# Kernel optimization log

Measured on AMD Instinct MI355X. Metric: run time of the kernel, lower is better.

The kernel has to match this reference:

```python
import jax, jax.numpy as jnp
import numpy as np

HIDDEN = 1024
HEADS = 16
HEAD_DIM = HIDDEN // HEADS


def setup_inputs() -> dict:
    key = jax.random.key(0)
    k_x, k_wa, k_ba, k_wp, k_bp = jax.random.split(key, 5)
    x = jax.random.normal(k_x, (2, 2048, HIDDEN), dtype=jnp.float32)
    s_a = 1.0 / np.sqrt(HIDDEN)
    # torch Linear default init ~ U(-1/sqrt(fan_in), 1/sqrt(fan_in)); stored as [in, out]
    W_attn = jax.random.uniform(k_wa, (HIDDEN, 3 * HIDDEN), jnp.float32, -s_a, s_a)
    b_attn = jax.random.uniform(k_ba, (3 * HIDDEN,), jnp.float32, -s_a, s_a)
    W_proj = jax.random.uniform(k_wp, (HIDDEN, HIDDEN), jnp.float32, -s_a, s_a)
    b_proj = jax.random.uniform(k_bp, (HIDDEN,), jnp.float32, -s_a, s_a)
    return {"x": x, "W_attn": W_attn, "b_attn": b_attn, "W_proj": W_proj, "b_proj": b_proj}


def reference(x, W_attn, b_attn, W_proj, b_proj):
    B, S, D = x.shape
    H, Hd = HEADS, HEAD_DIM
    qkv = x @ W_attn + b_attn                     # [B, S, 3D]
    q, k, v = jnp.split(qkv, 3, axis=-1)
    # [B, H, S, Hd]
    q = q.reshape(B, S, H, Hd).transpose(0, 2, 1, 3)
    k = k.reshape(B, S, H, Hd).transpose(0, 2, 1, 3)
    v = v.reshape(B, S, H, Hd).transpose(0, 2, 1, 3)
    scale = 1.0 / np.sqrt(Hd).astype(np.float32)
    scores = jnp.einsum('bhqd,bhkd->bhqk', q, k) * scale   # [B, H, S, S]
    causal = jnp.triu(jnp.ones((S, S), dtype=bool), k=1)   # True above diagonal
    scores = jnp.where(causal, -jnp.inf, scores)
    probs = jax.nn.softmax(scores, axis=-1)
    # dropout p=0.0 -> identity (eval-mode equivalent)
    ctx = jnp.einsum('bhqk,bhkd->bhqd', probs, v)           # [B, H, S, Hd]
    ctx = ctx.transpose(0, 2, 1, 3).reshape(B, S, D)
    return ctx @ W_proj + b_proj
```

## Files before the change

### kernel.cpp

```cpp
#include <hip/hip_runtime.h>
#include <hip/hip_bf16.h>
#include <stdint.h>

#define HID 1024
#define NH 16
#define HD 64
#define SEQ 2048
#define BATCH 2
#define M_TOT 4096
#define QSCALE 0.18033688011112042f

typedef __attribute__((ext_vector_type(8))) short short8;
typedef __attribute__((ext_vector_type(4))) float f32x4;
typedef __attribute__((ext_vector_type(16))) float f32x16;
typedef __hip_bfloat16 bf16;

__device__ __forceinline__ void load_lds16(const void* g, void* l) {
  __builtin_amdgcn_global_load_lds(
      (const __attribute__((address_space(1))) unsigned int*)g,
      (__attribute__((address_space(3))) unsigned int*)l, 16, 0, 0);
}

__device__ __forceinline__ unsigned short f2bf_bits(float f) {
  __hip_bfloat16 h = __float2bfloat16(f);
  return *reinterpret_cast<unsigned short*>(&h);
}
__device__ __forceinline__ unsigned pack2bf(float a, float b) {
  return (unsigned)f2bf_bits(a) | ((unsigned)f2bf_bits(b) << 16);
}
__device__ __forceinline__ unsigned cvt_pk_bf16(float a, float b) {
  unsigned r;
  asm("v_cvt_pk_bf16_f32 %0, %1, %2" : "=v"(r) : "v"(a), "v"(b));
  return r;
}

__global__ void cvt_f32_to_bf16(const float* __restrict__ in,
                                bf16* __restrict__ out, int n4) {
  int i = blockIdx.x * blockDim.x + threadIdx.x;
  if (i >= n4) return;
  float4 v = reinterpret_cast<const float4*>(in)[i];
  ushort4 o;
  o.x = f2bf_bits(v.x); o.y = f2bf_bits(v.y);
  o.z = f2bf_bits(v.z); o.w = f2bf_bits(v.w);
  reinterpret_cast<ushort4*>(out)[i] = o;
}

__global__ void transpose_cvt2(const float* __restrict__ Wa, bf16* __restrict__ WTa,
                               const float* __restrict__ Wp, bf16* __restrict__ WTp) {
  __shared__ float tile[32][33];
  int bx = blockIdx.x;
  const float* W; bf16* WT; int N;
  if (bx < 96) { W = Wa; WT = WTa; N = 3072; }
  else         { W = Wp; WT = WTp; N = 1024; bx -= 96; }
  const int K = 1024;
  int n0 = bx * 32, k0 = blockIdx.y * 32;
  int tx = threadIdx.x, ty = threadIdx.y;
#pragma unroll
  for (int i = 0; i < 32; i += 8)
    tile[ty + i][tx] = W[(size_t)(k0 + ty + i) * N + n0 + tx];
  __syncthreads();
#pragma unroll
  for (int i = 0; i < 32; i += 8)
    WT[(size_t)(n0 + ty + i) * K + k0 + tx] = __float2bfloat16(tile[tx][ty + i]);
}

template <int EPI>
__global__ __launch_bounds__(256, 2)
void gemm128(const bf16* __restrict__ A, const bf16* __restrict__ BT,
             const float* __restrict__ bias,
             bf16* __restrict__ Qo, bf16* __restrict__ Ko, bf16* __restrict__ Vo,
             float* __restrict__ Fo) {
  const int Kdim = 1024;
  __shared__ bf16 As[128 * 64];
  __shared__ bf16 Bs[128 * 64];
  const int tid = threadIdx.x;
  const int wid = tid >> 6, lane = tid & 63;
  const int m0 = blockIdx.x * 128;
  const int n0 = blockIdx.y * 128;
  const int wrow = (wid >> 1) * 64, wcol = (wid & 1) * 64;

  f32x4 acc[4][4];
#pragma unroll
  for (int rb = 0; rb < 4; ++rb)
#pragma unroll
    for (int cb = 0; cb < 4; ++cb)
      acc[rb][cb] = (f32x4){0.f, 0.f, 0.f, 0.f};

  const int lr = lane >> 3;
  const int cc = lane & 7;
  const int lc = cc * 8;
  const int fr = lane & 15, fk = (lane >> 4) * 8;

  for (int kt = 0; kt < Kdim / 64; ++kt) {
    __syncthreads();
#pragma unroll
    for (int t = 0; t < 4; ++t) {
      int i = wid * 4 + t;
      int row = i * 8 + lr;
      load_lds16(A + (size_t)(m0 + row) * Kdim + kt * 64 + lc, (char*)As + i * 1024);
      load_lds16(BT + (size_t)(n0 + row) * Kdim + kt * 64 + lc, (char*)Bs + i * 1024);
    }
    __syncthreads();

    short8 af[4][2], bf_[4][2];
#pragma unroll
    for (int rb = 0; rb < 4; ++rb)
#pragma unroll
      for (int kk = 0; kk < 2; ++kk) {
        af[rb][kk] = *(const short8*)&As[(wrow + rb * 16 + fr) * 64 + kk * 32 + fk];
        bf_[rb][kk] = *(const short8*)&Bs[(wcol + rb * 16 + fr) * 64 + kk * 32 + fk];
      }
#pragma unroll
    for (int rb = 0; rb < 4; ++rb)
#pragma unroll
      for (int cb = 0; cb < 4; ++cb)
#pragma unroll
        for (int kk = 0; kk < 2; ++kk)
          acc[rb][cb] = __builtin_amdgcn_mfma_f32_16x16x32_bf16(
              af[rb][kk], bf_[cb][kk], acc[rb][cb], 0, 0, 0);
  }

  const int fg = (lane >> 4) * 4;
  float bv[4];
#pragma unroll
  for (int cb = 0; cb < 4; ++cb) bv[cb] = bias[n0 + wcol + cb * 16 + fr];

  if (EPI == 0) {
    __syncthreads();
    char* ep = (wid < 2 ? (char*)As : (char*)Bs) + (wid & 1) * 8192;
    const int ncol = n0 + wcol;
    const int part = ncol >> 10;
    const int h = (ncol & 1023) >> 6;
    const int b = m0 >> 11;
    const int s_base = (m0 + wrow) & 2047;
    const size_t hb = (size_t)(b * NH + h);

    if (part < 2) {
      const float qs = (part == 0) ? QSCALE : 1.f;
#pragma unroll
      for (int rb = 0; rb < 4; ++rb)
#pragma unroll
        for (int cb = 0; cb < 4; ++cb)
#pragma unroll
          for (int j = 0; j < 4; ++j) {
            int row = rb * 16 + fg + j;
            int colb = (cb * 16 + fr) * 2;
            *(unsigned short*)(ep + row * 128 + (colb ^ ((row & 7) << 4))) =
                f2bf_bits((acc[rb][cb][j] + bv[cb]) * qs);
          }
      bf16* dst = (part == 0 ? Qo : Ko) + hb * SEQ * HD;
#pragma unroll
      for (int p = 0; p < 8; ++p) {
        int row = p * 8 + lr;
        uint4 v = *(const uint4*)(ep + row * 128 + ((cc * 16) ^ ((row & 7) << 4)));
        *(uint4*)(dst + (size_t)(s_base + row) * HD + cc * 8) = v;
      }
    } else {
#pragma unroll
      for (int rb = 0; rb < 4; ++rb)
#pragma unroll
        for (int cb = 0; cb < 4; ++cb) {
          int cV = cb * 16 + fr;
          int r0 = (rb * 16 + fg) * 2;
          uint2 wv;
          wv.x = pack2bf(acc[rb][cb][0] + bv[cb], acc[rb][cb][1] + bv[cb]);
          wv.y = pack2bf(acc[rb][cb][2] + bv[cb], acc[rb][cb][3] + bv[cb]);
          *(uint2*)(ep + cV * 128 + (r0 ^ ((cV & 7) << 4))) = wv;
        }
      bf16* dstV = Vo + hb * HD * SEQ;
#pragma unroll
      for (int p = 0; p < 8; ++p) {
        int hd = p * 8 + lr;
        uint4 v = *(const uint4*)(ep + hd * 128 + ((cc * 16) ^ ((hd & 7) << 4)));
        *(uint4*)(dstV + (size_t)hd * SEQ + s_base + cc * 8) = v;
      }
    }
  } else {
#pragma unroll
    for (int rb = 0; rb < 4; ++rb) {
      int r0 = m0 + wrow + rb * 16 + fg;
#pragma unroll
      for (int cb = 0; cb < 4; ++cb) {
        int n = n0 + wcol + cb * 16 + fr;
#pragma unroll
        for (int j = 0; j < 4; ++j)
          Fo[(size_t)(r0 + j) * HID + n] = acc[rb][cb][j] + bv[cb];
      }
    }
  }
}

__global__ __launch_bounds__(256, 2)
void attn_kernel(const bf16* __restrict__ Q, const bf16* __restrict__ K,
                 const bf16* __restrict__ VT, bf16* __restrict__ ctx) {
  __shared__ char smem[65536];
  const int tid = threadIdx.x, wid = tid >> 6, lane = tid & 63;
  const int idx = blockIdx.x;
  const int qt = (idx < 256) ? (15 - (idx >> 5)) : ((idx - 256) >> 5);
  const int bh = idx & 31;
  const int b = bh >> 4, h = bh & 15;
  const size_t base = (size_t)bh * SEQ * HD;
  const int q0 = qt * 128 + wid * 32;

  const int fr = lane & 31, hi = lane >> 5;
  const int lr = lane >> 3;
  const int cc = lane & 7;
  const int qg = q0 + fr;
  const int gc = (cc ^ lr) * 8;

  short8 qf[4];
  const bf16* qp = Q + base + (size_t)qg * HD;
#pragma unroll
  for (int kc = 0; kc < 4; ++kc)
    qf[kc] = *(const short8*)(qp + kc * 16 + hi * 8);

  f32x16 oa[2], ob[2];
#pragma unroll
  for (int da = 0; da < 2; ++da)
#pragma unroll
    for (int r = 0; r < 16; ++r) { oa[da][r] = 0.f; ob[da][r] = 0.f; }
  float lpart = 0.f;

  auto tile_compute = [&](const char* sb_t, int kv0, f32x16 (&oc)[2]) {
    f32x16 sa[2];
    __builtin_amdgcn_s_setprio(1);
#pragma unroll
    for (int kb = 0; kb < 2; ++kb) {
#pragma unroll
      for (int r = 0; r < 16; ++r) sa[kb][r] = 0.f;
      const int row = kb * 32 + fr;
      const int swz = (row & 7) << 4;
#pragma unroll
      for (int kc = 0; kc < 4; ++kc) {
        short8 kf = *(const short8*)(sb_t + row * 128 + ((kc * 32 + hi * 16) ^ swz));
        sa[kb] = __builtin_amdgcn_mfma_f32_32x32x16_bf16(kf, qf[kc], sa[kb], 0, 0, 0);
      }
    }
    __builtin_amdgcn_s_setprio(0);

    if (kv0 + 63 > q0) {
#pragma unroll
      for (int kb = 0; kb < 2; ++kb)
#pragma unroll
        for (int r = 0; r < 16; ++r) {
          int kvg = kv0 + kb * 32 + (r & 3) + 8 * (r >> 2) + 4 * hi;
          sa[kb][r] = (kvg > qg) ? -1e30f : sa[kb][r];
        }
    }

    float s0 = 0.f, s1 = 0.f, s2 = 0.f, s3 = 0.f;
#pragma unroll
    for (int kb = 0; kb < 2; ++kb)
#pragma unroll
      for (int r = 0; r < 16; ++r) {
        float e = __builtin_exp2f(sa[kb][r]);
        sa[kb][r] = e;
        if ((r & 3) == 0)      s0 += e;
        else if ((r & 3) == 1) s1 += e;
        else if ((r & 3) == 2) s2 += e;
        else                   s3 += e;
      }
    lpart += (s0 + s1) + (s2 + s3);

    unsigned pk[2][8], px[2][8];
#pragma unroll
    for (int kb = 0; kb < 2; ++kb) {
#pragma unroll
      for (int i = 0; i < 8; ++i)
        pk[kb][i] = cvt_pk_bf16(sa[kb][2 * i], sa[kb][2 * i + 1]);
#pragma unroll
      for (int i = 0; i < 8; ++i)
        px[kb][i] = (unsigned)__shfl_xor((int)pk[kb][i], 32);
    }

    __builtin_amdgcn_s_setprio(1);
#pragma unroll
    for (int da = 0; da < 2; ++da) {
      const int row = da * 32 + fr;
      const int swz = (row & 7) << 4;
#pragma unroll
      for (int ks = 0; ks < 4; ++ks) {
        short8 vf = *(const short8*)(sb_t + 8192 + row * 128 +
                                     ((ks * 32 + hi * 16) ^ swz));
        const int kb = ks >> 1, g = (ks & 1) * 4;
        union { unsigned u[4]; short8 s; } pf;
        pf.u[0] = hi ? px[kb][g + 2] : pk[kb][g + 0];
        pf.u[1] = hi ? px[kb][g + 3] : pk[kb][g + 1];
        pf.u[2] = hi ? pk[kb][g + 2] : px[kb][g + 0];
        pf.u[3] = hi ? pk[kb][g + 3] : px[kb][g + 1];
        oc[da] = __builtin_amdgcn_mfma_f32_32x32x16_bf16(vf, pf.s, oc[da], 0, 0, 0);
      }
    }
    __builtin_amdgcn_s_setprio(0);
  };

  const int npair = qt + 1;

#pragma unroll
  for (int u = 0; u < 2; ++u)
#pragma unroll
    for (int t = 0; t < 2; ++t) {
      int i = wid * 2 + t;
      load_lds16(K + base + (size_t)(u * 64 + i * 8 + lr) * HD + gc,
                 smem + u * 16384 + i * 1024);
      load_lds16(VT + base + (size_t)(i * 8 + lr) * SEQ + u * 64 + gc,
                 smem + u * 16384 + 8192 + i * 1024);
    }
  __syncthreads();

  for (int j = 0; j < npair; ++j) {
    char* sb = smem + (j & 1) * 32768;

    if (j + 1 < npair) {
      char* nb = smem + ((j + 1) & 1) * 32768;
      const int nv = (j + 1) * 128;
#pragma unroll
      for (int u = 0; u < 2; ++u)
#pragma unroll
        for (int t = 0; t < 2; ++t) {
          int i = wid * 2 + t;
          load_lds16(K + base + (size_t)(nv + u * 64 + i * 8 + lr) * HD + gc,
                     nb + u * 16384 + i * 1024);
          load_lds16(VT + base + (size_t)(i * 8 + lr) * SEQ + nv + u * 64 + gc,
                     nb + u * 16384 + 8192 + i * 1024);
        }
    }

    const int kv0 = j * 128;
    if (kv0 <= q0 + 31)      tile_compute(sb,         kv0,      oa);
    if (kv0 + 64 <= q0 + 31) tile_compute(sb + 16384, kv0 + 64, ob);

    __syncthreads();
  }

  const float lrun = lpart + __shfl_xor(lpart, 32);
  const float inv = 1.f / lrun;
  char* ep = smem + wid * 4096;
#pragma unroll
  for (int da = 0; da < 2; ++da)
#pragma unroll
    for (int rg = 0; rg < 4; ++rg) {
      int d0 = da * 64 + rg * 16 + hi * 8;
      float v0 = (oa[da][rg * 4 + 0] + ob[da][rg * 4 + 0]) * inv;
      float v1 = (oa[da][rg * 4 + 1] + ob[da][rg * 4 + 1]) * inv;
      float v2 = (oa[da][rg * 4 + 2] + ob[da][rg * 4 + 2]) * inv;
      float v3 = (oa[da][rg * 4 + 3] + ob[da][rg * 4 + 3]) * inv;
      uint2 wv; wv.x = pack2bf(v0, v1); wv.y = pack2bf(v2, v3);
      *(uint2*)(ep + fr * 128 + (d0 ^ ((fr & 7) << 4))) = wv;
    }
#pragma unroll
  for (int p = 0; p < 4; ++p) {
    int qr = p * 8 + lr;
    uint4 v = *(const uint4*)(ep + qr * 128 + ((cc * 16) ^ ((qr & 7) << 4)));
    int s = q0 + qr;
    *(uint4*)(ctx + (size_t)(b * SEQ + s) * HID + h * 64 + cc * 8) = v;
  }
}

extern "C" void kernel_launch(void* const* d_in, const int* in_sizes, int n_in,
                              void* d_out, int out_size, void* d_ws, size_t ws_size,
                              hipStream_t stream) {
  const float* x      = (const float*)d_in[0];
  const float* W_attn = (const float*)d_in[1];
  const float* b_attn = (const float*)d_in[2];
  const float* W_proj = (const float*)d_in[3];
  const float* b_proj = (const float*)d_in[4];
  float* out = (float*)d_out;

  char* ws = (char*)d_ws;
  const size_t MB = 1u << 20;
  bf16* xb   = (bf16*)(ws + 0);
  bf16* WTa  = (bf16*)(ws + 8 * MB);
  bf16* WTp  = (bf16*)(ws + 14 * MB);
  bf16* Qw   = (bf16*)(ws + 16 * MB);
  bf16* Kw   = (bf16*)(ws + 24 * MB);
  bf16* VTw  = (bf16*)(ws + 32 * MB);
  bf16* ctxb = (bf16*)(ws + 40 * MB);

  cvt_f32_to_bf16<<<(M_TOT * HID / 4 + 255) / 256, 256, 0, stream>>>(x, xb, M_TOT * HID / 4);
  transpose_cvt2<<<dim3(128, 32), dim3(32, 8), 0, stream>>>(W_attn, WTa, W_proj, WTp);

  gemm128<0><<<dim3(M_TOT / 128, 3 * HID / 128), 256, 0, stream>>>(
      xb, WTa, b_attn, Qw, Kw, VTw, nullptr);

  attn_kernel<<<dim3(512), 256, 0, stream>>>(Qw, Kw, VTw, ctxb);

  gemm128<1><<<dim3(M_TOT / 128, HID / 128), 256, 0, stream>>>(
      ctxb, WTp, b_proj, nullptr, nullptr, nullptr, out);
}
```

Baseline: 113.8 us.

## Load K/V fragments directly from global into registers, drop LDS staging

The attention kernel no longer stages K and V^T tiles in double-buffered LDS with block-wide barriers. Each wave now loads its MFMA operand fragments straight from global memory into registers, prefetching K one tile ahead, and walks only the tiles its own causal range needs. The bf16 P fragment exchange uses permlane32_swap instead of shfl_xor plus selects. This removes the __syncthreads barriers and LDS traffic. In exchange, the four waves of a block each fetch the same K/V data separately (relying on cache), register pressure rises, and the V loads are not prefetched.

Measured after the change: 135.3 us. 18.9% more time.

```diff
diff --git a/kernel.cpp b/kernel.cpp
--- a/kernel.cpp
+++ b/kernel.cpp
@@ -193,7 +193,7 @@
 __global__ __launch_bounds__(256, 2)
 void attn_kernel(const bf16* __restrict__ Q, const bf16* __restrict__ K,
                  const bf16* __restrict__ VT, bf16* __restrict__ ctx) {
-  __shared__ char smem[65536];
+  __shared__ char smem[16384];
   const int tid = threadIdx.x, wid = tid >> 6, lane = tid & 63;
   const int idx = blockIdx.x;
   const int qt = (idx < 256) ? (15 - (idx >> 5)) : ((idx - 256) >> 5);
@@ -206,7 +206,9 @@
   const int lr = lane >> 3;
   const int cc = lane & 7;
   const int qg = q0 + fr;
-  const int gc = (cc ^ lr) * 8;
+
+  const bf16* Kp = K + base;
+  const bf16* Vp = VT + base;
 
   short8 qf[4];
   const bf16* qp = Q + base + (size_t)qg * HD;
@@ -221,20 +223,35 @@
     for (int r = 0; r < 16; ++r) { oa[da][r] = 0.f; ob[da][r] = 0.f; }
   float lpart = 0.f;
 
-  auto tile_compute = [&](const char* sb_t, int kv0, f32x16 (&oc)[2]) {
+  auto loadK = [&](int kv0, short8 (&kf)[2][4]) {
+#pragma unroll
+    for (int kb = 0; kb < 2; ++kb)
+#pragma unroll
+      for (int kc = 0; kc < 4; ++kc)
+        kf[kb][kc] = *(const short8*)(Kp + (size_t)(kv0 + kb * 32 + fr) * HD +
+                                      kc * 16 + hi * 8);
+  };
+  auto loadV = [&](int kv0, short8 (&vf)[2][4]) {
+#pragma unroll
+    for (int da = 0; da < 2; ++da)
+#pragma unroll
+      for (int ks = 0; ks < 4; ++ks)
+        vf[da][ks] = *(const short8*)(Vp + (size_t)(da * 32 + fr) * SEQ + kv0 +
+                                      ks * 16 + hi * 8);
+  };
+
+  auto tile_compute = [&](short8 (&kf)[2][4], short8 (&vf)[2][4], int kv0,
+                          f32x16 (&oc)[2]) {
     f32x16 sa[2];
     __builtin_amdgcn_s_setprio(1);
 #pragma unroll
     for (int kb = 0; kb < 2; ++kb) {
 #pragma unroll
       for (int r = 0; r < 16; ++r) sa[kb][r] = 0.f;
-      const int row = kb * 32 + fr;
-      const int swz = (row & 7) << 4;
-#pragma unroll
-      for (int kc = 0; kc < 4; ++kc) {
-        short8 kf = *(const short8*)(sb_t + row * 128 + ((kc * 32 + hi * 16) ^ swz));
-        sa[kb] = __builtin_amdgcn_mfma_f32_32x32x16_bf16(kf, qf[kc], sa[kb], 0, 0, 0);
-      }
+#pragma unroll
+      for (int kc = 0; kc < 4; ++kc)
+        sa[kb] = __builtin_amdgcn_mfma_f32_32x32x16_bf16(kf[kb][kc], qf[kc],
+                                                         sa[kb], 0, 0, 0);
     }
     __builtin_amdgcn_s_setprio(0);
 
@@ -262,75 +279,51 @@
       }
     lpart += (s0 + s1) + (s2 + s3);
 
-    unsigned pk[2][8], px[2][8];
-#pragma unroll
-    for (int kb = 0; kb < 2; ++kb) {
+    unsigned pk[2][8];
+#pragma unroll
+    for (int kb = 0; kb < 2; ++kb)
 #pragma unroll
       for (int i = 0; i < 8; ++i)
         pk[kb][i] = cvt_pk_bf16(sa[kb][2 * i], sa[kb][2 * i + 1]);
-#pragma unroll
-      for (int i = 0; i < 8; ++i)
-        px[kb][i] = (unsigned)__shfl_xor((int)pk[kb][i], 32);
+
+    short8 pfr[4];
+#pragma unroll
+    for (int ks = 0; ks < 4; ++ks) {
+      const int kb = ks >> 1, g = (ks & 1) * 4;
+      auto r0 = __builtin_amdgcn_permlane32_swap((int)pk[kb][g + 0],
+                                                 (int)pk[kb][g + 2], false, false);
+      auto r1 = __builtin_amdgcn_permlane32_swap((int)pk[kb][g + 1],
+                                                 (int)pk[kb][g + 3], false, false);
+      union { unsigned u[4]; short8 s; } pf;
+      pf.u[0] = (unsigned)r0[0]; pf.u[1] = (unsigned)r1[0];
+      pf.u[2] = (unsigned)r0[1]; pf.u[3] = (unsigned)r1[1];
+      pfr[ks] = pf.s;
     }
 
     __builtin_amdgcn_s_setprio(1);
 #pragma unroll
-    for (int da = 0; da < 2; ++da) {
-      const int row = da * 32 + fr;
-      const int swz = (row & 7) << 4;
-#pragma unroll
-      for (int ks = 0; ks < 4; ++ks) {
-        short8 vf = *(const short8*)(sb_t + 8192 + row * 128 +
-                                     ((ks * 32 + hi * 16) ^ swz));
-        const int kb = ks >> 1, g = (ks & 1) * 4;
-        union { unsigned u[4]; short8 s; } pf;
-        pf.u[0] = hi ? px[kb][g + 2] : pk[kb][g + 0];
-        pf.u[1] = hi ? px[kb][g + 3] : pk[kb][g + 1];
-        pf.u[2] = hi ? pk[kb][g + 2] : px[kb][g + 0];
-        pf.u[3] = hi ? pk[kb][g + 3] : px[kb][g + 1];
-        oc[da] = __builtin_amdgcn_mfma_f32_32x32x16_bf16(vf, pf.s, oc[da], 0, 0, 0);
-      }
-    }
+    for (int da = 0; da < 2; ++da)
+#pragma unroll
+      for (int ks = 0; ks < 4; ++ks)
+        oc[da] = __builtin_amdgcn_mfma_f32_32x32x16_bf16(vf[da][ks], pfr[ks],
+                                                         oc[da], 0, 0, 0);
     __builtin_amdgcn_s_setprio(0);
   };
 
-  const int npair = qt + 1;
-
-#pragma unroll
-  for (int u = 0; u < 2; ++u)
-#pragma unroll
-    for (int t = 0; t < 2; ++t) {
-      int i = wid * 2 + t;
-      load_lds16(K + base + (size_t)(u * 64 + i * 8 + lr) * HD + gc,
-                 smem + u * 16384 + i * 1024);
-      load_lds16(VT + base + (size_t)(i * 8 + lr) * SEQ + u * 64 + gc,
-                 smem + u * 16384 + 8192 + i * 1024);
-    }
-  __syncthreads();
-
-  for (int j = 0; j < npair; ++j) {
-    char* sb = smem + (j & 1) * 32768;
-
-    if (j + 1 < npair) {
-      char* nb = smem + ((j + 1) & 1) * 32768;
-      const int nv = (j + 1) * 128;
-#pragma unroll
-      for (int u = 0; u < 2; ++u)
-#pragma unroll
-        for (int t = 0; t < 2; ++t) {
-          int i = wid * 2 + t;
-          load_lds16(K + base + (size_t)(nv + u * 64 + i * 8 + lr) * HD + gc,
-                     nb + u * 16384 + i * 1024);
-          load_lds16(VT + base + (size_t)(i * 8 + lr) * SEQ + nv + u * 64 + gc,
-                     nb + u * 16384 + 8192 + i * 1024);
-        }
-    }
-
-    const int kv0 = j * 128;
-    if (kv0 <= q0 + 31)      tile_compute(sb,         kv0,      oa);
-    if (kv0 + 64 <= q0 + 31) tile_compute(sb + 16384, kv0 + 64, ob);
-
-    __syncthreads();
+  const int ntiles = ((q0 + 31) >> 6) + 1;
+  short8 kE[2][4], vE[2][4], kO[2][4], vO[2][4];
+  loadK(0, kE);
+  if (ntiles > 1) loadK(64, kO);
+
+  for (int t = 0; t < ntiles; t += 2) {
+    loadV(t * 64, vE);
+    tile_compute(kE, vE, t * 64, oa);
+    if (t + 2 < ntiles) loadK((t + 2) * 64, kE);
+    if (t + 1 < ntiles) {
+      loadV((t + 1) * 64, vO);
+      tile_compute(kO, vO, (t + 1) * 64, ob);
+      if (t + 3 < ntiles) loadK((t + 3) * 64, kO);
+    }
   }
 
   const float lrun = lpart + __shfl_xor(lpart, 32);
```

## Replace shuffles with permlane32_swap and use explicit vmcnt waits in KV pipeline

Applied to the files above, without the earlier changes.

The P fragment exchange between wave halves now uses permlane32_swap instead of eight ds_bpermute-style __shfl_xor calls per block plus lane-dependent selects, which removes LDS shuffle traffic and VALU selects. The K/V staging loop is restructured so the next tile's global-to-LDS loads are issued first, followed by a partial s_waitcnt vmcnt(8) that waits only for the current tile. Raw s_barrier calls replace __syncthreads, letting the prefetch stay in flight during compute. The hand-written waitcnt counts have to match the number of issued loads exactly, otherwise the ordering becomes fragile.

Result: faster. 109.3 us (-4.0%).

```diff
diff --git a/kernel.cpp b/kernel.cpp
--- a/kernel.cpp
+++ b/kernel.cpp
@@ -221,6 +221,21 @@
     for (int r = 0; r < 16; ++r) { oa[da][r] = 0.f; ob[da][r] = 0.f; }
   float lpart = 0.f;
 
+  auto stage_pair = [&](int jp) {
+    char* nb = smem + (jp & 1) * 32768;
+    const int nv = jp * 128;
+#pragma unroll
+    for (int u = 0; u < 2; ++u)
+#pragma unroll
+      for (int t = 0; t < 2; ++t) {
+        int i = wid * 2 + t;
+        load_lds16(K + base + (size_t)(nv + u * 64 + i * 8 + lr) * HD + gc,
+                   nb + u * 16384 + i * 1024);
+        load_lds16(VT + base + (size_t)(i * 8 + lr) * SEQ + nv + u * 64 + gc,
+                   nb + u * 16384 + 8192 + i * 1024);
+      }
+  };
+
   auto tile_compute = [&](const char* sb_t, int kv0, f32x16 (&oc)[2]) {
     f32x16 sa[2];
     __builtin_amdgcn_s_setprio(1);
@@ -262,15 +277,25 @@
       }
     lpart += (s0 + s1) + (s2 + s3);
 
-    unsigned pk[2][8], px[2][8];
-#pragma unroll
-    for (int kb = 0; kb < 2; ++kb) {
+    unsigned pk[2][8];
+#pragma unroll
+    for (int kb = 0; kb < 2; ++kb)
 #pragma unroll
       for (int i = 0; i < 8; ++i)
         pk[kb][i] = cvt_pk_bf16(sa[kb][2 * i], sa[kb][2 * i + 1]);
-#pragma unroll
-      for (int i = 0; i < 8; ++i)
-        px[kb][i] = (unsigned)__shfl_xor((int)pk[kb][i], 32);
+
+    short8 pfr[4];
+#pragma unroll
+    for (int ks = 0; ks < 4; ++ks) {
+      const int kb = ks >> 1, g = (ks & 1) * 4;
+      auto r0 = __builtin_amdgcn_permlane32_swap((int)pk[kb][g + 0],
+                                                 (int)pk[kb][g + 2], false, false);
+      auto r1 = __builtin_amdgcn_permlane32_swap((int)pk[kb][g + 1],
+                                                 (int)pk[kb][g + 3], false, false);
+      union { unsigned u[4]; short8 s; } pf;
+      pf.u[0] = (unsigned)r0[0]; pf.u[1] = (unsigned)r1[0];
+      pf.u[2] = (unsigned)r0[1]; pf.u[3] = (unsigned)r1[1];
+      pfr[ks] = pf.s;
     }
 
     __builtin_amdgcn_s_setprio(1);
@@ -282,13 +307,7 @@
       for (int ks = 0; ks < 4; ++ks) {
         short8 vf = *(const short8*)(sb_t + 8192 + row * 128 +
                                      ((ks * 32 + hi * 16) ^ swz));
-        const int kb = ks >> 1, g = (ks & 1) * 4;
-        union { unsigned u[4]; short8 s; } pf;
-        pf.u[0] = hi ? px[kb][g + 2] : pk[kb][g + 0];
-        pf.u[1] = hi ? px[kb][g + 3] : pk[kb][g + 1];
-        pf.u[2] = hi ? pk[kb][g + 2] : px[kb][g + 0];
-        pf.u[3] = hi ? pk[kb][g + 3] : px[kb][g + 1];
-        oc[da] = __builtin_amdgcn_mfma_f32_32x32x16_bf16(vf, pf.s, oc[da], 0, 0, 0);
+        oc[da] = __builtin_amdgcn_mfma_f32_32x32x16_bf16(vf, pfr[ks], oc[da], 0, 0, 0);
       }
     }
     __builtin_amdgcn_s_setprio(0);
@@ -296,41 +315,28 @@
 
   const int npair = qt + 1;
 
-#pragma unroll
-  for (int u = 0; u < 2; ++u)
-#pragma unroll
-    for (int t = 0; t < 2; ++t) {
-      int i = wid * 2 + t;
-      load_lds16(K + base + (size_t)(u * 64 + i * 8 + lr) * HD + gc,
-                 smem + u * 16384 + i * 1024);
-      load_lds16(VT + base + (size_t)(i * 8 + lr) * SEQ + u * 64 + gc,
-                 smem + u * 16384 + 8192 + i * 1024);
-    }
-  __syncthreads();
+  stage_pair(0);
 
   for (int j = 0; j < npair; ++j) {
     char* sb = smem + (j & 1) * 32768;
 
+    __builtin_amdgcn_s_barrier();
+    __builtin_amdgcn_sched_barrier(0);
+
     if (j + 1 < npair) {
-      char* nb = smem + ((j + 1) & 1) * 32768;
-      const int nv = (j + 1) * 128;
-#pragma unroll
-      for (int u = 0; u < 2; ++u)
-#pragma unroll
-        for (int t = 0; t < 2; ++t) {
-          int i = wid * 2 + t;
-          load_lds16(K + base + (size_t)(nv + u * 64 + i * 8 + lr) * HD + gc,
-                     nb + u * 16384 + i * 1024);
-          load_lds16(VT + base + (size_t)(i * 8 + lr) * SEQ + nv + u * 64 + gc,
-                     nb + u * 16384 + 8192 + i * 1024);
-        }
-    }
+      stage_pair(j + 1);
+      asm volatile("s_waitcnt vmcnt(8)" ::: "memory");
+    } else {
+      asm volatile("s_waitcnt vmcnt(0)" ::: "memory");
+    }
+    __builtin_amdgcn_sched_barrier(0);
+
+    __builtin_amdgcn_s_barrier();
+    __builtin_amdgcn_sched_barrier(0);
 
     const int kv0 = j * 128;
     if (kv0 <= q0 + 31)      tile_compute(sb,         kv0,      oa);
     if (kv0 + 64 <= q0 + 31) tile_compute(sb + 16384, kv0 + 64, ob);
-
-    __syncthreads();
   }
 
   const float lrun = lpart + __shfl_xor(lpart, 32);
```
